# Kernel optimization log

Hardware: AMD Instinct MI355X
Metric: run time of the kernel (lower is better)

Reference implementation:

```python
import jax, jax.numpy as jnp
import numpy as np

N, E, G = 65536, 524288, 1024
ND, ED, HID, H, C = 21, 12, 128, 4, 32
L = 8  # num_blocks * 2 conv layers
EPS = 1e-5


def _gatv2(x, src, dst, ea, Wl, Wr, We, att, bias):
    # PyG GATv2Conv: xl=lin_l(x) (source), xr=lin_r(x) (target)
    n = x.shape[0]
    xl = jnp.einsum('nd,dhc->nhc', x, Wl)   # [N,H,C]
    xr = jnp.einsum('nd,dhc->nhc', x, Wr)
    el = jnp.einsum('ed,dhc->ehc', ea, We)  # [E,H,C]
    m = xl[src] + xr[dst] + el              # per-edge message pre-activation
    e = jnp.einsum('ehc,hc->eh', jax.nn.leaky_relu(m, 0.2), att)  # [E,H]
    # scatter softmax over incoming edges of each dst node
    emax = jax.ops.segment_max(e, dst, num_segments=n)
    emax = jnp.where(jnp.isfinite(emax), emax, 0.0)
    p = jnp.exp(e - emax[dst])
    denom = jax.ops.segment_sum(p, dst, num_segments=n)
    alpha = p / jnp.clip(denom, 1e-16)[dst]
    out = jax.ops.segment_sum(alpha[..., None] * xl[src], dst, num_segments=n)
    return out.reshape(n, H * C) + bias


def _bn(x, scale, bias):
    mu = x.mean(0)
    var = x.var(0)
    return (x - mu) * jax.lax.rsqrt(var + EPS) * scale + bias


def setup_inputs():
    key = jax.random.key(0)
    ks = jax.random.split(key, 16)
    f = lambda k, shp, s=0.05: jax.random.normal(k, shp, jnp.float32) * s
    return dict(
        x=f(ks[0], (N, ND), 1.0),
        edge_attr=f(ks[1], (E, ED), 1.0),
        edge_index=jax.random.randint(ks[2], (2, E), 0, N),
        batch=jnp.sort(jax.random.randint(ks[3], (N,), 0, G)),
        Win=f(ks[4], (ND, HID)), bin_=jnp.zeros(HID),
        Wl=f(ks[5], (L, HID, H, C)), Wr=f(ks[6], (L, HID, H, C)),
        We=f(ks[7], (L, ED, H, C)), att=f(ks[8], (L, H, C)),
        bconv=jnp.zeros((L, HID)),
        bn_scale=jnp.ones((L, HID)), bn_bias=jnp.zeros((L, HID)),
        Wv1=f(ks[9], (HID, 64)), bv1=jnp.zeros(64),
        Wv2=f(ks[10], (64, 3)), bv2=jnp.zeros(3),
        Wp1=f(ks[11], (2 * HID + ED, 64)), bp1=jnp.zeros(64),
        Wp2=f(ks[12], (64, 1)), bp2=jnp.zeros(1),
    )


def reference(x, edge_attr, edge_index, batch, Win, bin_, Wl, Wr, We, att,
              bconv, bn_scale, bn_bias, Wv1, bv1, Wv2, bv2, Wp1, bp1, Wp2, bp2):
    src0, dst0 = edge_index[0], edge_index[1]
    # add_self_loops with fill_value='mean' for edge features
    ones_e = jnp.ones((E,), x.dtype)
    deg = jax.ops.segment_sum(ones_e, dst0, num_segments=N)
    mean_ea = jax.ops.segment_sum(edge_attr, dst0, num_segments=N) / jnp.clip(deg, 1.0)[:, None]
    ar = jnp.arange(N)
    src = jnp.concatenate([src0, ar])
    dst = jnp.concatenate([dst0, ar])
    ea = jnp.concatenate([edge_attr, mean_ea], axis=0)

    h = jax.nn.relu(x @ Win + bin_)
    for b in range(L // 2):
        i, j = 2 * b, 2 * b + 1
        res = h
        h = _gatv2(h, src, dst, ea, Wl[i], Wr[i], We[i], att[i], bconv[i])
        h = jax.nn.relu(_bn(h, bn_scale[i], bn_bias[i]))
        h = _gatv2(h, src, dst, ea, Wl[j], Wr[j], We[j], att[j], bconv[j])
        h = _bn(h, bn_scale[j], bn_bias[j])
        h = jax.nn.relu(h + res)

    counts = jax.ops.segment_sum(jnp.ones((N,), h.dtype), batch, num_segments=G)
    pooled = jax.ops.segment_sum(h, batch, num_segments=G) / jnp.clip(counts, 1.0)[:, None]
    value_logits = jax.nn.relu(pooled @ Wv1 + bv1) @ Wv2 + bv2  # [G,3]

    edge_input = jnp.concatenate([h[src0], h[dst0], edge_attr], axis=1)  # [E, 2*HID+ED]
    policy_logits = (jax.nn.relu(edge_input @ Wp1 + bp1) @ Wp2 + bp2)[:, 0]  # [E]
    return value_logits, policy_logits
```

## Files before the change

### kernel.cpp

```cpp
#include <hip/hip_runtime.h>
#include <hip/hip_fp16.h>

#define NN 65536
#define EE 524288
#define EPX 589824
#define GG 1024
#define NSLOT 32

typedef __attribute__((ext_vector_type(8))) short bf16x8;
typedef __attribute__((ext_vector_type(4))) float f32x4;

#define LOG2E 1.44269504088896f


__device__ __forceinline__ unsigned short f2bf(float x) {
    unsigned int u = __float_as_uint(x);
    u += 0x7FFFu + ((u >> 16) & 1u);
    return (unsigned short)(u >> 16);
}
__device__ __forceinline__ float bflo(unsigned int w) { return __uint_as_float(w << 16); }
__device__ __forceinline__ float bfhi(unsigned int w) { return __uint_as_float(w & 0xFFFF0000u); }
__device__ __forceinline__ float bf2f(unsigned short u) { return __uint_as_float((unsigned int)u << 16); }
__device__ __forceinline__ float lrelu(float x) { return fmaf(0.4f, fabsf(x), 0.6f * x); }
__device__ __forceinline__ unsigned int packh2(float a, float b) {
    __half2 h = __floats2half2_rn(a, b);
    return *reinterpret_cast<unsigned int*>(&h);
}
__device__ __forceinline__ unsigned long long rfl64(unsigned long long v) {
    unsigned int lo = __builtin_amdgcn_readfirstlane((unsigned int)v);
    unsigned int hi = __builtin_amdgcn_readfirstlane((unsigned int)(v >> 32));
    return (((unsigned long long)hi) << 32) | lo;
}


__launch_bounds__(256)
__global__ void k_deg(const int* __restrict__ dst0, int* __restrict__ deg)
{
    int e = blockIdx.x * 256 + threadIdx.x;
    if (e >= EE) return;
    atomicAdd(&deg[dst0[e]], 1);
}

__launch_bounds__(1024)
__global__ void k_scan(const int* __restrict__ deg, int* __restrict__ rowptr)
{
    __shared__ int sums[1024];
    int t = threadIdx.x;
    int base = t * 64;
    int s = 0;
    for (int i = 0; i < 64; i++) s += deg[base + i] + 1;
    sums[t] = s;
    __syncthreads();
    for (int off = 1; off < 1024; off <<= 1) {
        int v = (t >= off) ? sums[t - off] : 0;
        __syncthreads();
        sums[t] += v;
        __syncthreads();
    }
    int off = sums[t] - s;
    for (int i = 0; i < 64; i++) { rowptr[base + i] = off; off += deg[base + i] + 1; }
    if (t == 1023) rowptr[NN] = off;
}

__launch_bounds__(256)
__global__ void k_scatter(const int* __restrict__ src0, const int* __restrict__ dst0,
                          const float* __restrict__ eattr,
                          const int* __restrict__ rowptr, const int* __restrict__ deg,
                          int* __restrict__ fill, int* __restrict__ csr_src,
                          unsigned short* __restrict__ eaCSR)
{
    int e = blockIdx.x * 256 + threadIdx.x;
    if (e >= EPX) return;
    if (e < EE) {
        int d = dst0[e];
        int pos = rowptr[d] + atomicAdd(&fill[d], 1);
        csr_src[pos] = src0[e] << 8;
        const float* ep = eattr + (size_t)e * 12;
        float4 a = *reinterpret_cast<const float4*>(ep);
        float4 b = *reinterpret_cast<const float4*>(ep + 4);
        float4 c = *reinterpret_cast<const float4*>(ep + 8);
        uint2* q = reinterpret_cast<uint2*>(eaCSR + (size_t)pos * 12);
        q[0] = make_uint2(packh2(a.x, a.y), packh2(a.z, a.w));
        q[1] = make_uint2(packh2(b.x, b.y), packh2(b.z, b.w));
        q[2] = make_uint2(packh2(c.x, c.y), packh2(c.z, c.w));
    } else {
        int n = e - EE;
        csr_src[rowptr[n] + deg[n]] = n << 8;
    }
}

__launch_bounds__(256)
__global__ void k_selfattr(const int* __restrict__ rowptr, unsigned short* __restrict__ eaCSR)
{
    int tid = blockIdx.x * 256 + threadIdx.x;
    int n = tid >> 4;
    int lk = tid & 15;
    if (lk >= 12) return;
    int beg = rowptr[n], endm1 = rowptr[n + 1] - 1;
    float s = 0.f;
    for (int p = beg; p < endm1; ++p) {
        __half h = *reinterpret_cast<const __half*>(&eaCSR[(size_t)p * 12 + lk]);
        s += __half2float(h);
    }
    float dv = fmaxf((float)(endm1 - beg), 1.0f);
    __half ho = __float2half(s / dv);
    eaCSR[(size_t)endm1 * 12 + lk] = *reinterpret_cast<unsigned short*>(&ho);
}


__launch_bounds__(256)
__global__ void k_wprep(const float* __restrict__ Wl, const float* __restrict__ Wr,
                        const float* __restrict__ Wp1,
                        unsigned short* __restrict__ wg, unsigned short* __restrict__ wp)
{
    int tid = blockIdx.x * 256 + threadIdx.x;
    if (tid < 32768) {
        int l = tid >> 12;
        int r = tid & 4095;
        int kt = r >> 10, ct = (r >> 6) & 15, lane = r & 63;
        int kb = kt * 32 + (lane >> 4) * 8;
        int col = ct * 16 + (lane & 15);
        const float* W = (col < 128) ? (Wl + (size_t)l * 16384 + col)
                                     : (Wr + (size_t)l * 16384 + (col - 128));
        unsigned short* o = wg + (size_t)tid * 8;
#pragma unroll
        for (int j = 0; j < 8; j++) o[j] = f2bf(W[(size_t)(kb + j) * 128]);
    } else if (tid < 34816) {
        int r = tid - 32768;
        int kt = r >> 9, ct = (r >> 6) & 7, lane = r & 63;
        int kb = kt * 32 + (lane >> 4) * 8;
        int col = ct * 16 + (lane & 15);
        const float* W = (col < 64) ? (Wp1 + col) : (Wp1 + 128 * 64 + (col - 64));
        unsigned short* o = wp + (size_t)r * 8;
#pragma unroll
        for (int j = 0; j < 8; j++) o[j] = f2bf(W[(size_t)(kb + j) * 64]);
    }
}


__launch_bounds__(256)
__global__ void k_input(const float* __restrict__ x, const float* __restrict__ Win,
                        const float* __restrict__ bin, float* __restrict__ h)
{
    __shared__ float W[21 * 128];
    int t = threadIdx.x;
    for (int i = t; i < 21 * 128; i += 256) W[i] = Win[i];
    __syncthreads();
    int c = t & 127, sub = t >> 7;
    int n0 = blockIdx.x * 16;
    float bc = bin[c];
    for (int i = 0; i < 8; i++) {
        int n = n0 + sub + i * 2;
        const float* xp = x + (size_t)n * 21;
        float acc = bc;
#pragma unroll
        for (int k = 0; k < 21; k++) acc = fmaf(xp[k], W[k * 128 + c], acc);
        h[(size_t)n * 128 + c] = fmaxf(acc, 0.f);
    }
}


__device__ __forceinline__ void load_afrag(const float* __restrict__ A, int arow, int kb,
                                           bf16x8 af[4])
{
#pragma unroll
    for (int kt = 0; kt < 4; kt++) {
        const float* ap = A + (size_t)arow * 128 + kt * 32 + kb;
        float4 lo = *reinterpret_cast<const float4*>(ap);
        float4 hi = *reinterpret_cast<const float4*>(ap + 4);
        bf16x8 v;
        v[0] = (short)f2bf(lo.x); v[1] = (short)f2bf(lo.y);
        v[2] = (short)f2bf(lo.z); v[3] = (short)f2bf(lo.w);
        v[4] = (short)f2bf(hi.x); v[5] = (short)f2bf(hi.y);
        v[6] = (short)f2bf(hi.z); v[7] = (short)f2bf(hi.w);
        af[kt] = v;
    }
}

__device__ __forceinline__ void gemm_gat_core(const bf16x8 af[4], const unsigned short* __restrict__ Bf,
                                              int row0, unsigned short* __restrict__ Cl,
                                              unsigned short* __restrict__ Cr, int lane)
{
    int crow = row0 + (lane >> 4) * 4;
    int c0 = lane & 15;
#pragma unroll
    for (int ct = 0; ct < 16; ct++) {
        f32x4 acc = {0.f, 0.f, 0.f, 0.f};
#pragma unroll
        for (int kt = 0; kt < 4; kt++) {
            bf16x8 bf = *reinterpret_cast<const bf16x8*>(Bf + ((size_t)(kt * 16 + ct) * 64 + lane) * 8);
            acc = __builtin_amdgcn_mfma_f32_16x16x32_bf16(af[kt], bf, acc, 0, 0, 0);
        }
        int col = ct * 16 + c0;
        unsigned short* C = (col < 128) ? Cl : Cr;
        int cc = col & 127;
#pragma unroll
        for (int r = 0; r < 4; r++)
            C[(size_t)(crow + r) * 128 + cc] = f2bf(acc[r]);
    }
}

__launch_bounds__(256)
__global__ void k_gemm_gat(const float* __restrict__ A, const unsigned short* __restrict__ Bf,
                           unsigned short* __restrict__ Cl, unsigned short* __restrict__ Cr)
{
    int wave = threadIdx.x >> 6, lane = threadIdx.x & 63;
    int row0 = blockIdx.x * 64 + wave * 16;
    bf16x8 af[4];
    load_afrag(A, row0 + (lane & 15), (lane >> 4) * 8, af);
    gemm_gat_core(af, Bf, row0, Cl, Cr, lane);
}

__launch_bounds__(256)
__global__ void k_gemm_gat_bn(const float* __restrict__ G, const float* __restrict__ bnstat,
                              const float* __restrict__ scale, const float* __restrict__ bias,
                              const unsigned short* __restrict__ Bf,
                              unsigned short* __restrict__ Cl, unsigned short* __restrict__ Cr)
{
    __shared__ float sA[128], bA[128];
    int t = threadIdx.x;
    if (t < 128) {
        float sum = 0.f, sq = 0.f;
#pragma unroll
        for (int sl = 0; sl < NSLOT; sl++) {
            sum += bnstat[sl * 256 + t];
            sq  += bnstat[sl * 256 + 128 + t];
        }
        const float invN = 1.0f / (float)NN;
        float mean = sum * invN;
        float var  = sq * invN - mean * mean;
        float sc   = scale[t] * rsqrtf(var + 1e-5f);
        sA[t] = sc;
        bA[t] = bias[t] - mean * sc;
    }
    __syncthreads();
    int wave = t >> 6, lane = t & 63;
    int row0 = blockIdx.x * 64 + wave * 16;
    int arow = row0 + (lane & 15);
    int kb = (lane >> 4) * 8;
    bf16x8 af[4];
#pragma unroll
    for (int kt = 0; kt < 4; kt++) {
        int cb = kt * 32 + kb;
        const float* gp = G + (size_t)arow * 128 + cb;
        float4 lo = *reinterpret_cast<const float4*>(gp);
        float4 hi = *reinterpret_cast<const float4*>(gp + 4);
        bf16x8 v;
        v[0] = (short)f2bf(fmaxf(fmaf(lo.x, sA[cb + 0], bA[cb + 0]), 0.f));
        v[1] = (short)f2bf(fmaxf(fmaf(lo.y, sA[cb + 1], bA[cb + 1]), 0.f));
        v[2] = (short)f2bf(fmaxf(fmaf(lo.z, sA[cb + 2], bA[cb + 2]), 0.f));
        v[3] = (short)f2bf(fmaxf(fmaf(lo.w, sA[cb + 3], bA[cb + 3]), 0.f));
        v[4] = (short)f2bf(fmaxf(fmaf(hi.x, sA[cb + 4], bA[cb + 4]), 0.f));
        v[5] = (short)f2bf(fmaxf(fmaf(hi.y, sA[cb + 5], bA[cb + 5]), 0.f));
        v[6] = (short)f2bf(fmaxf(fmaf(hi.z, sA[cb + 6], bA[cb + 6]), 0.f));
        v[7] = (short)f2bf(fmaxf(fmaf(hi.w, sA[cb + 7], bA[cb + 7]), 0.f));
        af[kt] = v;
    }
    gemm_gat_core(af, Bf, row0, Cl, Cr, lane);
}

__launch_bounds__(256)
__global__ void k_gemm_pol(const float* __restrict__ A, const unsigned short* __restrict__ Bf,
                           unsigned short* __restrict__ P)
{
    int wave = threadIdx.x >> 6, lane = threadIdx.x & 63;
    int row0 = blockIdx.x * 64 + wave * 16;
    bf16x8 af[4];
    load_afrag(A, row0 + (lane & 15), (lane >> 4) * 8, af);
    int crow = row0 + (lane >> 4) * 4;
    int c0 = lane & 15;
#pragma unroll
    for (int ct = 0; ct < 8; ct++) {
        f32x4 acc = {0.f, 0.f, 0.f, 0.f};
#pragma unroll
        for (int kt = 0; kt < 4; kt++) {
            bf16x8 bf = *reinterpret_cast<const bf16x8*>(Bf + ((size_t)(kt * 8 + ct) * 64 + lane) * 8);
            acc = __builtin_amdgcn_mfma_f32_16x16x32_bf16(af[kt], bf, acc, 0, 0, 0);
        }
        int col = ct * 16 + c0;
#pragma unroll
        for (int r = 0; r < 4; r++)
            P[(size_t)(crow + r) * 128 + col] = f2bf(acc[r]);
    }
}


__device__ __forceinline__ float2 edge_el(uint2 qa, uint2 qb, uint2 qc,
                                          const __half2 wx[6], const __half2 wy[6])
{
    __half2 e0 = *reinterpret_cast<const __half2*>(&qa.x);
    __half2 e1 = *reinterpret_cast<const __half2*>(&qa.y);
    __half2 e2 = *reinterpret_cast<const __half2*>(&qb.x);
    __half2 e3 = *reinterpret_cast<const __half2*>(&qb.y);
    __half2 e4 = *reinterpret_cast<const __half2*>(&qc.x);
    __half2 e5 = *reinterpret_cast<const __half2*>(&qc.y);
    __half2 ax = __hmul2(e0, wx[0]);
    ax = __hfma2(e1, wx[1], ax); ax = __hfma2(e2, wx[2], ax);
    ax = __hfma2(e3, wx[3], ax); ax = __hfma2(e4, wx[4], ax);
    ax = __hfma2(e5, wx[5], ax);
    __half2 ay = __hmul2(e0, wy[0]);
    ay = __hfma2(e1, wy[1], ay); ay = __hfma2(e2, wy[2], ay);
    ay = __hfma2(e3, wy[3], ay); ay = __hfma2(e4, wy[4], ay);
    ay = __hfma2(e5, wy[5], ay);
    float2 r;
    r.x = __half2float(__hadd(__low2half(ax), __high2half(ax)));
    r.y = __half2float(__hadd(__low2half(ay), __high2half(ay)));
    return r;
}

__device__ __forceinline__ float head_reduce(float t)
{
    t += __shfl_xor(t, 1);
    t += __shfl_xor(t, 2);
    t += __shfl_xor(t, 4);
    t += __shfl_xor(t, 8);
    return t;
}

__launch_bounds__(256)
__global__ void k_gat(const unsigned short* __restrict__ xlb, const unsigned short* __restrict__ xrb,
                      const unsigned short* __restrict__ eaCSR,
                      const int* __restrict__ rowptr, const int* __restrict__ csr_src,
                      const float* __restrict__ We, const float* __restrict__ att,
                      const float* __restrict__ bconv, float* __restrict__ g,
                      float* __restrict__ bnstat)
{
    int wid = blockIdx.x * 4 + (threadIdx.x >> 6);
    int lane = threadIdx.x & 63;
    int f0 = lane * 2;

    const int* cs_s = (const int*)rfl64((unsigned long long)csr_src);
    const unsigned short* ea_s = (const unsigned short*)rfl64((unsigned long long)eaCSR);

    __half2 wx[6], wy[6];
#pragma unroll
    for (int j = 0; j < 6; j++) {
        float2 w0 = *reinterpret_cast<const float2*>(We + (2 * j) * 128 + f0);
        float2 w1 = *reinterpret_cast<const float2*>(We + (2 * j + 1) * 128 + f0);
        wx[j] = __floats2half2_rn(w0.x, w1.x);
        wy[j] = __floats2half2_rn(w0.y, w1.y);
    }
    float2 av = *reinterpret_cast<const float2*>(att + f0);
    av.x *= LOG2E; av.y *= LOG2E;
    float2 bc = *reinterpret_cast<const float2*>(bconv + f0);
    const char* xl_lane = reinterpret_cast<const char*>(xlb) + (lane << 2);

    float bs0 = 0.f, bs1 = 0.f, bq0 = 0.f, bq1 = 0.f;

    for (int n = wid * 4; n < wid * 4 + 4; ++n) {
        unsigned int xrw = *reinterpret_cast<const unsigned int*>(xrb + (size_t)n * 128 + f0);
        float xr0 = bflo(xrw), xr1 = bfhi(xrw);

        float m = -INFINITY, s = 0.f, a0 = 0.f, a1 = 0.f;
        int beg = rowptr[n], end = rowptr[n + 1];
        int idx = beg;
        for (; idx + 4 <= end; idx += 4) {
            int off0 = cs_s[idx],     off1 = cs_s[idx + 1];
            int off2 = cs_s[idx + 2], off3 = cs_s[idx + 3];
            const uint2* q = reinterpret_cast<const uint2*>(ea_s + (size_t)idx * 12);
            uint2 qa = q[0], qb = q[1],  qc = q[2];
            uint2 ra = q[3], rb = q[4],  rc = q[5];
            uint2 sa = q[6], sb = q[7],  sc = q[8];
            uint2 ta = q[9], tb = q[10], tc = q[11];
            unsigned int xw0 = *reinterpret_cast<const unsigned int*>(xl_lane + off0);
            unsigned int xw1 = *reinterpret_cast<const unsigned int*>(xl_lane + off1);
            unsigned int xw2 = *reinterpret_cast<const unsigned int*>(xl_lane + off2);
            unsigned int xw3 = *reinterpret_cast<const unsigned int*>(xl_lane + off3);

            float2 el0 = edge_el(qa, qb, qc, wx, wy);
            float2 el1 = edge_el(ra, rb, rc, wx, wy);
            float2 el2 = edge_el(sa, sb, sc, wx, wy);
            float2 el3 = edge_el(ta, tb, tc, wx, wy);

            float xa0 = bflo(xw0), xa1 = bfhi(xw0);
            float xb0 = bflo(xw1), xb1 = bfhi(xw1);
            float xc0 = bflo(xw2), xc1 = bfhi(xw2);
            float xd0 = bflo(xw3), xd1 = bfhi(xw3);

            float t0 = lrelu(xa0 + xr0 + el0.x) * av.x + lrelu(xa1 + xr1 + el0.y) * av.y;
            float t1 = lrelu(xb0 + xr0 + el1.x) * av.x + lrelu(xb1 + xr1 + el1.y) * av.y;
            float t2 = lrelu(xc0 + xr0 + el2.x) * av.x + lrelu(xc1 + xr1 + el2.y) * av.y;
            float t3 = lrelu(xd0 + xr0 + el3.x) * av.x + lrelu(xd1 + xr1 + el3.y) * av.y;
            t0 = head_reduce(t0); t1 = head_reduce(t1);
            t2 = head_reduce(t2); t3 = head_reduce(t3);

            float nm = fmaxf(fmaxf(fmaxf(t0, t1), fmaxf(t2, t3)), m);
            float so = exp2f(m - nm);
            float w0 = exp2f(t0 - nm);
            float w1 = exp2f(t1 - nm);
            float w2 = exp2f(t2 - nm);
            float w3 = exp2f(t3 - nm);
            s  = fmaf(s, so, (w0 + w1) + (w2 + w3));
            a0 = fmaf(a0, so, fmaf(w0, xa0, fmaf(w1, xb0, fmaf(w2, xc0, w3 * xd0))));
            a1 = fmaf(a1, so, fmaf(w0, xa1, fmaf(w1, xb1, fmaf(w2, xc1, w3 * xd1))));
            m = nm;
        }
        for (; idx < end; ++idx) {
            int off0 = cs_s[idx];
            const uint2* q = reinterpret_cast<const uint2*>(ea_s + (size_t)idx * 12);
            uint2 qa = q[0], qb = q[1], qc = q[2];
            unsigned int xw0 = *reinterpret_cast<const unsigned int*>(xl_lane + off0);
            float2 el0 = edge_el(qa, qb, qc, wx, wy);
            float xa0 = bflo(xw0), xa1 = bfhi(xw0);
            float tt = lrelu(xa0 + xr0 + el0.x) * av.x + lrelu(xa1 + xr1 + el0.y) * av.y;
            tt = head_reduce(tt);
            float nm = fmaxf(m, tt);
            float so = exp2f(m - nm);
            float w  = exp2f(tt - nm);
            s  = fmaf(s, so, w);
            a0 = fmaf(a0, so, w * xa0);
            a1 = fmaf(a1, so, w * xa1);
            m = nm;
        }
        float inv = 1.f / s;
        float r0 = fmaf(a0, inv, bc.x);
        float r1 = fmaf(a1, inv, bc.y);
        *reinterpret_cast<float2*>(g + (size_t)n * 128 + f0) = make_float2(r0, r1);
        bs0 += r0; bs1 += r1;
        bq0 = fmaf(r0, r0, bq0); bq1 = fmaf(r1, r1, bq1);
    }

    __shared__ float red[256 * 4];
    int t = threadIdx.x;
    red[t * 4 + 0] = bs0; red[t * 4 + 1] = bs1;
    red[t * 4 + 2] = bq0; red[t * 4 + 3] = bq1;
    __syncthreads();
    if (t < 64) {
        float v0 = red[t * 4 + 0] + red[(t + 64) * 4 + 0] + red[(t + 128) * 4 + 0] + red[(t + 192) * 4 + 0];
        float v1 = red[t * 4 + 1] + red[(t + 64) * 4 + 1] + red[(t + 128) * 4 + 1] + red[(t + 192) * 4 + 1];
        float q0 = red[t * 4 + 2] + red[(t + 64) * 4 + 2] + red[(t + 128) * 4 + 2] + red[(t + 192) * 4 + 2];
        float q1 = red[t * 4 + 3] + red[(t + 64) * 4 + 3] + red[(t + 128) * 4 + 3] + red[(t + 192) * 4 + 3];
        float* slot = bnstat + (size_t)(blockIdx.x & (NSLOT - 1)) * 256;
        atomicAdd(&slot[2 * t + 0], v0);
        atomicAdd(&slot[2 * t + 1], v1);
        atomicAdd(&slot[128 + 2 * t + 0], q0);
        atomicAdd(&slot[128 + 2 * t + 1], q1);
    }
}


__launch_bounds__(256)
__global__ void k_bnapply_res_relu(const float4* __restrict__ gin,
                                   const float* __restrict__ bnstat,
                                   const float* __restrict__ scale, const float* __restrict__ bias,
                                   float4* __restrict__ hbuf)
{
    __shared__ float sA[128], bA[128];
    int t = threadIdx.x;
    if (t < 128) {
        float sum = 0.f, sq = 0.f;
#pragma unroll
        for (int sl = 0; sl < NSLOT; sl++) {
            sum += bnstat[sl * 256 + t];
            sq  += bnstat[sl * 256 + 128 + t];
        }
        const float invN = 1.0f / (float)NN;
        float mean = sum * invN;
        float var  = sq * invN - mean * mean;
        float sc   = scale[t] * rsqrtf(var + 1e-5f);
        sA[t] = sc;
        bA[t] = bias[t] - mean * sc;
    }
    __syncthreads();
    int idx = blockIdx.x * 256 + t;
    int c4 = (idx & 31) * 4;
    float4 v = gin[idx];
    float4 hv = hbuf[idx];
    float4 r;
    r.x = fmaxf(fmaf(v.x, sA[c4 + 0], bA[c4 + 0]) + hv.x, 0.f);
    r.y = fmaxf(fmaf(v.y, sA[c4 + 1], bA[c4 + 1]) + hv.y, 0.f);
    r.z = fmaxf(fmaf(v.z, sA[c4 + 2], bA[c4 + 2]) + hv.z, 0.f);
    r.w = fmaxf(fmaf(v.w, sA[c4 + 3], bA[c4 + 3]) + hv.w, 0.f);
    hbuf[idx] = r;
}


__launch_bounds__(128)
__global__ void k_pool(const float* __restrict__ h, const int* __restrict__ batch,
                       float* __restrict__ pooled, float* __restrict__ cnt)
{
    int c = threadIdx.x;
    int r0 = blockIdx.x * 128;
    int cur = batch[r0];
    float acc = 0.f;
    float run = 0.f;
    for (int i = 0; i < 128; ++i) {
        int r = r0 + i;
        int b = batch[r];
        if (b != cur) {
            atomicAdd(&pooled[(size_t)cur * 128 + c], acc);
            if (c == 0) atomicAdd(&cnt[cur], run);
            acc = 0.f; run = 0.f; cur = b;
        }
        acc += h[(size_t)r * 128 + c];
        run += 1.f;
    }
    atomicAdd(&pooled[(size_t)cur * 128 + c], acc);
    if (c == 0) atomicAdd(&cnt[cur], run);
}

__launch_bounds__(64)
__global__ void k_value(const float* __restrict__ pooled, const float* __restrict__ cnt,
                        const float* __restrict__ Wv1, const float* __restrict__ bv1,
                        const float* __restrict__ Wv2, const float* __restrict__ bv2,
                        float* __restrict__ out)
{
    int gi = blockIdx.x;
    int l = threadIdx.x;
    float inv = 1.f / fmaxf(cnt[gi], 1.f);
    const float* pr = pooled + (size_t)gi * 128;
    float z = bv1[l];
    for (int k = 0; k < 128; k++) z = fmaf(pr[k] * inv, Wv1[k * 64 + l], z);
    z = fmaxf(z, 0.f);
#pragma unroll
    for (int j = 0; j < 3; j++) {
        float p = z * Wv2[l * 3 + j];
        p += __shfl_xor(p, 32); p += __shfl_xor(p, 16); p += __shfl_xor(p, 8);
        p += __shfl_xor(p, 4);  p += __shfl_xor(p, 2);  p += __shfl_xor(p, 1);
        if (l == 0) out[gi * 3 + j] = p + bv2[j];
    }
}


__launch_bounds__(256)
__global__ void k_policy(const unsigned short* __restrict__ P,
                         const float* __restrict__ eattr,
                         const int* __restrict__ src0, const int* __restrict__ dst0,
                         const float* __restrict__ Wp1c, const float* __restrict__ bp1,
                         const float* __restrict__ Wp2, const float* __restrict__ bp2,
                         float* __restrict__ out)
{
    int wave = (blockIdx.x * 256 + threadIdx.x) >> 6;
    int lane = threadIdx.x & 63;
    const float* ea_s = (const float*)rfl64((unsigned long long)eattr);
    const int* s_s = (const int*)rfl64((unsigned long long)src0);
    const int* d_s = (const int*)rfl64((unsigned long long)dst0);
    float w1c[12];
#pragma unroll
    for (int k = 0; k < 12; k++) w1c[k] = Wp1c[k * 64 + lane];
    float wp2 = Wp2[lane];
    float bb = bp1[lane];
    float b2 = bp2[0];
    for (int i = 0; i < 8; i++) {
        int e = wave * 8 + i;
        int sI = s_s[e], dI = d_s[e];
        const float* ep = ea_s + (size_t)e * 12;
        float4 e0 = *reinterpret_cast<const float4*>(ep);
        float4 e1 = *reinterpret_cast<const float4*>(ep + 4);
        float4 e2 = *reinterpret_cast<const float4*>(ep + 8);
        float z = bf2f(P[(size_t)sI * 128 + lane]) + bf2f(P[(size_t)dI * 128 + 64 + lane]) + bb;
        z += e0.x * w1c[0] + e0.y * w1c[1] + e0.z * w1c[2]  + e0.w * w1c[3]
           + e1.x * w1c[4] + e1.y * w1c[5] + e1.z * w1c[6]  + e1.w * w1c[7]
           + e2.x * w1c[8] + e2.y * w1c[9] + e2.z * w1c[10] + e2.w * w1c[11];
        z = fmaxf(z, 0.f);
        float p = z * wp2;
        p += __shfl_xor(p, 32); p += __shfl_xor(p, 16); p += __shfl_xor(p, 8);
        p += __shfl_xor(p, 4);  p += __shfl_xor(p, 2);  p += __shfl_xor(p, 1);
        if (lane == 0) out[3072 + e] = p + b2;
    }
}


extern "C" void kernel_launch(void* const* d_in, const int* in_sizes, int n_in,
                              void* d_out, int out_size, void* d_ws, size_t ws_size,
                              hipStream_t stream)
{
    const float* x     = (const float*)d_in[0];
    const float* eattr = (const float*)d_in[1];
    const int*   eidx  = (const int*)d_in[2];
    const int*   batch = (const int*)d_in[3];
    const float* Win   = (const float*)d_in[4];
    const float* bin   = (const float*)d_in[5];
    const float* Wl    = (const float*)d_in[6];
    const float* Wr    = (const float*)d_in[7];
    const float* We    = (const float*)d_in[8];
    const float* att   = (const float*)d_in[9];
    const float* bconv = (const float*)d_in[10];
    const float* bnsc  = (const float*)d_in[11];
    const float* bnbi  = (const float*)d_in[12];
    const float* Wv1   = (const float*)d_in[13];
    const float* bv1   = (const float*)d_in[14];
    const float* Wv2   = (const float*)d_in[15];
    const float* bv2   = (const float*)d_in[16];
    const float* Wp1   = (const float*)d_in[17];
    const float* bp1   = (const float*)d_in[18];
    const float* Wp2   = (const float*)d_in[19];
    const float* bp2   = (const float*)d_in[20];
    float* out = (float*)d_out;

    const int* src0 = eidx;
    const int* dst0 = eidx + EE;

    const size_t NH = (size_t)NN * 128;
    float* ws = (float*)d_ws;
    float* h  = ws;
    float* g  = h + NH;
    unsigned short* xlb = (unsigned short*)(g + NH);
    unsigned short* xrb = xlb + NH;
    unsigned short* eaCSR = xrb + NH;
    int* rowptr = (int*)(eaCSR + (size_t)EPX * 12);
    int* csr_src = rowptr + (NN + 1);
    int* deg  = csr_src + EPX;
    int* fill = deg + NN;
    float* bnstat = (float*)(fill + NN);
    float* pooled = bnstat + 8 * NSLOT * 256;
    float* cnt    = pooled + (size_t)GG * 128;
    size_t zero_elems = (size_t)NN + NN + 8 * NSLOT * 256 + (size_t)GG * 128 + GG;
    unsigned short* wg = (unsigned short*)(cnt + GG);
    unsigned short* wp = wg + 8 * 32768;

    hipMemsetAsync(deg, 0, zero_elems * sizeof(float), stream);

    k_deg<<<EE / 256, 256, 0, stream>>>(dst0, deg);
    k_scan<<<1, 1024, 0, stream>>>(deg, rowptr);
    k_scatter<<<EPX / 256, 256, 0, stream>>>(src0, dst0, eattr, rowptr, deg, fill, csr_src, eaCSR);
    k_selfattr<<<(NN * 16) / 256, 256, 0, stream>>>(rowptr, eaCSR);
    k_wprep<<<136, 256, 0, stream>>>(Wl, Wr, Wp1, wg, wp);

    k_input<<<NN / 16, 256, 0, stream>>>(x, Win, bin, h);

    for (int l = 0; l < 8; l++) {
        float* bs = bnstat + (size_t)l * NSLOT * 256;
        if (l % 2 == 0) {
            k_gemm_gat<<<NN / 64, 256, 0, stream>>>(h, wg + (size_t)l * 32768, xlb, xrb);
        } else {
            float* bsp = bnstat + (size_t)(l - 1) * NSLOT * 256;
            k_gemm_gat_bn<<<NN / 64, 256, 0, stream>>>(g, bsp,
                                                       bnsc + (size_t)(l - 1) * 128,
                                                       bnbi + (size_t)(l - 1) * 128,
                                                       wg + (size_t)l * 32768, xlb, xrb);
        }
        k_gat<<<NN / 16, 256, 0, stream>>>(xlb, xrb, eaCSR, rowptr, csr_src,
                                           We + (size_t)l * 1536, att + (size_t)l * 128,
                                           bconv + (size_t)l * 128, g, bs);
        if (l % 2 == 1) {
            k_bnapply_res_relu<<<(NN * 128 / 4) / 256, 256, 0, stream>>>(
                (const float4*)g, bs, bnsc + (size_t)l * 128, bnbi + (size_t)l * 128,
                (float4*)h);
        }
    }

    k_pool<<<NN / 128, 128, 0, stream>>>(h, batch, pooled, cnt);
    k_value<<<GG, 64, 0, stream>>>(pooled, cnt, Wv1, bv1, Wv2, bv2, out);

    unsigned short* P = xlb;
    k_gemm_pol<<<NN / 64, 256, 0, stream>>>(h, wp, P);
    k_policy<<<NN / 4, 256, 0, stream>>>(P, eattr, src0, dst0,
                                         Wp1 + 256 * 64, bp1, Wp2, bp2, out);
}
```

Before: 1.146 ms.

## Split GAT layer into edge-parallel logit kernel and node-parallel aggregation kernel

Moves the per-edge attention logit computation into its own edge-parallel kernel, where each wave handles a fixed chunk of 64 CSR edges and writes per-head logits to a scratch buffer. The aggregation kernel then reads precomputed logits and only gathers source features for the online softmax. The aim is to remove the load imbalance that variable node degree causes in the fused per-node loop. In exchange it adds a csr_dst array, a second gather of xl per edge, an extra launch, and a logit write plus read-back each layer.

Measured after the change: 1.246 ms. 1.09x slower.

```diff
diff --git a/kernel.cpp b/kernel.cpp
--- a/kernel.cpp
+++ b/kernel.cpp
@@ -67,7 +67,7 @@
                           const float* __restrict__ eattr,
                           const int* __restrict__ rowptr, const int* __restrict__ deg,
                           int* __restrict__ fill, int* __restrict__ csr_src,
-                          unsigned short* __restrict__ eaCSR)
+                          int* __restrict__ csr_dst, unsigned short* __restrict__ eaCSR)
 {
     int e = blockIdx.x * 256 + threadIdx.x;
     if (e >= EPX) return;
@@ -75,6 +75,7 @@
         int d = dst0[e];
         int pos = rowptr[d] + atomicAdd(&fill[d], 1);
         csr_src[pos] = src0[e] << 8;
+        csr_dst[pos] = d << 8;
         const float* ep = eattr + (size_t)e * 12;
         float4 a = *reinterpret_cast<const float4*>(ep);
         float4 b = *reinterpret_cast<const float4*>(ep + 4);
@@ -85,7 +86,9 @@
         q[2] = make_uint2(packh2(c.x, c.y), packh2(c.z, c.w));
     } else {
         int n = e - EE;
-        csr_src[rowptr[n] + deg[n]] = n << 8;
+        int pos = rowptr[n] + deg[n];
+        csr_src[pos] = n << 8;
+        csr_dst[pos] = n << 8;
     }
 }
 
@@ -318,19 +321,17 @@
 }
 
 __launch_bounds__(256)
-__global__ void k_gat(const unsigned short* __restrict__ xlb, const unsigned short* __restrict__ xrb,
-                      const unsigned short* __restrict__ eaCSR,
-                      const int* __restrict__ rowptr, const int* __restrict__ csr_src,
-                      const float* __restrict__ We, const float* __restrict__ att,
-                      const float* __restrict__ bconv, float* __restrict__ g,
-                      float* __restrict__ bnstat)
+__global__ void k_logit(const unsigned short* __restrict__ xlb, const unsigned short* __restrict__ xrb,
+                        const unsigned short* __restrict__ eaCSR,
+                        const int* __restrict__ csr_src, const int* __restrict__ csr_dst,
+                        const float* __restrict__ We, const float* __restrict__ att,
+                        float* __restrict__ tlog)
 {
     int wid = blockIdx.x * 4 + (threadIdx.x >> 6);
     int lane = threadIdx.x & 63;
     int f0 = lane * 2;
-
-    const int* cs_s = (const int*)rfl64((unsigned long long)csr_src);
-    const unsigned short* ea_s = (const unsigned short*)rfl64((unsigned long long)eaCSR);
+    int head = lane >> 4;
+    bool wl = (lane & 15) == 0;
 
     __half2 wx[6], wy[6];
 #pragma unroll
@@ -342,47 +343,83 @@
     }
     float2 av = *reinterpret_cast<const float2*>(att + f0);
     av.x *= LOG2E; av.y *= LOG2E;
+    const char* xl_lane = reinterpret_cast<const char*>(xlb) + (lane << 2);
+    const char* xr_lane = reinterpret_cast<const char*>(xrb) + (lane << 2);
+
+    int p0 = wid * 64;
+    for (int p = p0; p < p0 + 64; p += 4) {
+        int so0 = csr_src[p],     so1 = csr_src[p + 1];
+        int so2 = csr_src[p + 2], so3 = csr_src[p + 3];
+        int do0 = csr_dst[p],     do1 = csr_dst[p + 1];
+        int do2 = csr_dst[p + 2], do3 = csr_dst[p + 3];
+        const uint2* q = reinterpret_cast<const uint2*>(eaCSR + (size_t)p * 12);
+        uint2 qa = q[0], qb = q[1],  qc = q[2];
+        uint2 ra = q[3], rb = q[4],  rc = q[5];
+        uint2 sa = q[6], sb = q[7],  sc = q[8];
+        uint2 ta = q[9], tb = q[10], tc = q[11];
+        unsigned int xs0 = *reinterpret_cast<const unsigned int*>(xl_lane + so0);
+        unsigned int xs1 = *reinterpret_cast<const unsigned int*>(xl_lane + so1);
+        unsigned int xs2 = *reinterpret_cast<const unsigned int*>(xl_lane + so2);
+        unsigned int xs3 = *reinterpret_cast<const unsigned int*>(xl_lane + so3);
+        unsigned int xd0 = *reinterpret_cast<const unsigned int*>(xr_lane + do0);
+        unsigned int xd1 = *reinterpret_cast<const unsigned int*>(xr_lane + do1);
+        unsigned int xd2 = *reinterpret_cast<const unsigned int*>(xr_lane + do2);
+        unsigned int xd3 = *reinterpret_cast<const unsigned int*>(xr_lane + do3);
+
+        float2 el0 = edge_el(qa, qb, qc, wx, wy);
+        float2 el1 = edge_el(ra, rb, rc, wx, wy);
+        float2 el2 = edge_el(sa, sb, sc, wx, wy);
+        float2 el3 = edge_el(ta, tb, tc, wx, wy);
+
+        float t0 = lrelu(bflo(xs0) + bflo(xd0) + el0.x) * av.x + lrelu(bfhi(xs0) + bfhi(xd0) + el0.y) * av.y;
+        float t1 = lrelu(bflo(xs1) + bflo(xd1) + el1.x) * av.x + lrelu(bfhi(xs1) + bfhi(xd1) + el1.y) * av.y;
+        float t2 = lrelu(bflo(xs2) + bflo(xd2) + el2.x) * av.x + lrelu(bfhi(xs2) + bfhi(xd2) + el2.y) * av.y;
+        float t3 = lrelu(bflo(xs3) + bflo(xd3) + el3.x) * av.x + lrelu(bfhi(xs3) + bfhi(xd3) + el3.y) * av.y;
+        t0 = head_reduce(t0); t1 = head_reduce(t1);
+        t2 = head_reduce(t2); t3 = head_reduce(t3);
+
+        if (wl) {
+            tlog[(size_t)(p + 0) * 4 + head] = t0;
+            tlog[(size_t)(p + 1) * 4 + head] = t1;
+            tlog[(size_t)(p + 2) * 4 + head] = t2;
+            tlog[(size_t)(p + 3) * 4 + head] = t3;
+        }
+    }
+}
+
+
+__launch_bounds__(256)
+__global__ void k_gat2(const unsigned short* __restrict__ xlb,
+                       const float* __restrict__ tlog,
+                       const int* __restrict__ rowptr, const int* __restrict__ csr_src,
+                       const float* __restrict__ bconv, float* __restrict__ g,
+                       float* __restrict__ bnstat)
+{
+    int wid = blockIdx.x * 4 + (threadIdx.x >> 6);
+    int lane = threadIdx.x & 63;
+    int f0 = lane * 2;
+    int head = lane >> 4;
     float2 bc = *reinterpret_cast<const float2*>(bconv + f0);
     const char* xl_lane = reinterpret_cast<const char*>(xlb) + (lane << 2);
+    const float* tl = tlog + head;
 
     float bs0 = 0.f, bs1 = 0.f, bq0 = 0.f, bq1 = 0.f;
 
     for (int n = wid * 4; n < wid * 4 + 4; ++n) {
-        unsigned int xrw = *reinterpret_cast<const unsigned int*>(xrb + (size_t)n * 128 + f0);
-        float xr0 = bflo(xrw), xr1 = bfhi(xrw);
-
         float m = -INFINITY, s = 0.f, a0 = 0.f, a1 = 0.f;
         int beg = rowptr[n], end = rowptr[n + 1];
         int idx = beg;
         for (; idx + 4 <= end; idx += 4) {
-            int off0 = cs_s[idx],     off1 = cs_s[idx + 1];
-            int off2 = cs_s[idx + 2], off3 = cs_s[idx + 3];
-            const uint2* q = reinterpret_cast<const uint2*>(ea_s + (size_t)idx * 12);
-            uint2 qa = q[0], qb = q[1],  qc = q[2];
-            uint2 ra = q[3], rb = q[4],  rc = q[5];
-            uint2 sa = q[6], sb = q[7],  sc = q[8];
-            uint2 ta = q[9], tb = q[10], tc = q[11];
+            int off0 = csr_src[idx],     off1 = csr_src[idx + 1];
+            int off2 = csr_src[idx + 2], off3 = csr_src[idx + 3];
+            float t0 = tl[(size_t)(idx + 0) * 4];
+            float t1 = tl[(size_t)(idx + 1) * 4];
+            float t2 = tl[(size_t)(idx + 2) * 4];
+            float t3 = tl[(size_t)(idx + 3) * 4];
             unsigned int xw0 = *reinterpret_cast<const unsigned int*>(xl_lane + off0);
             unsigned int xw1 = *reinterpret_cast<const unsigned int*>(xl_lane + off1);
             unsigned int xw2 = *reinterpret_cast<const unsigned int*>(xl_lane + off2);
             unsigned int xw3 = *reinterpret_cast<const unsigned int*>(xl_lane + off3);
-
-            float2 el0 = edge_el(qa, qb, qc, wx, wy);
-            float2 el1 = edge_el(ra, rb, rc, wx, wy);
-            float2 el2 = edge_el(sa, sb, sc, wx, wy);
-            float2 el3 = edge_el(ta, tb, tc, wx, wy);
-
-            float xa0 = bflo(xw0), xa1 = bfhi(xw0);
-            float xb0 = bflo(xw1), xb1 = bfhi(xw1);
-            float xc0 = bflo(xw2), xc1 = bfhi(xw2);
-            float xd0 = bflo(xw3), xd1 = bfhi(xw3);
-
-            float t0 = lrelu(xa0 + xr0 + el0.x) * av.x + lrelu(xa1 + xr1 + el0.y) * av.y;
-            float t1 = lrelu(xb0 + xr0 + el1.x) * av.x + lrelu(xb1 + xr1 + el1.y) * av.y;
-            float t2 = lrelu(xc0 + xr0 + el2.x) * av.x + lrelu(xc1 + xr1 + el2.y) * av.y;
-            float t3 = lrelu(xd0 + xr0 + el3.x) * av.x + lrelu(xd1 + xr1 + el3.y) * av.y;
-            t0 = head_reduce(t0); t1 = head_reduce(t1);
-            t2 = head_reduce(t2); t3 = head_reduce(t3);
 
             float nm = fmaxf(fmaxf(fmaxf(t0, t1), fmaxf(t2, t3)), m);
             float so = exp2f(m - nm);
@@ -390,23 +427,23 @@
             float w1 = exp2f(t1 - nm);
             float w2 = exp2f(t2 - nm);
             float w3 = exp2f(t3 - nm);
+            float xa0 = bflo(xw0), xa1 = bfhi(xw0);
+            float xb0 = bflo(xw1), xb1 = bfhi(xw1);
+            float xc0 = bflo(xw2), xc1 = bfhi(xw2);
+            float xd0 = bflo(xw3), xd1 = bfhi(xw3);
             s  = fmaf(s, so, (w0 + w1) + (w2 + w3));
             a0 = fmaf(a0, so, fmaf(w0, xa0, fmaf(w1, xb0, fmaf(w2, xc0, w3 * xd0))));
             a1 = fmaf(a1, so, fmaf(w0, xa1, fmaf(w1, xb1, fmaf(w2, xc1, w3 * xd1))));
             m = nm;
         }
         for (; idx < end; ++idx) {
-            int off0 = cs_s[idx];
-            const uint2* q = reinterpret_cast<const uint2*>(ea_s + (size_t)idx * 12);
-            uint2 qa = q[0], qb = q[1], qc = q[2];
+            int off0 = csr_src[idx];
+            float tt = tl[(size_t)idx * 4];
             unsigned int xw0 = *reinterpret_cast<const unsigned int*>(xl_lane + off0);
-            float2 el0 = edge_el(qa, qb, qc, wx, wy);
-            float xa0 = bflo(xw0), xa1 = bfhi(xw0);
-            float tt = lrelu(xa0 + xr0 + el0.x) * av.x + lrelu(xa1 + xr1 + el0.y) * av.y;
-            tt = head_reduce(tt);
             float nm = fmaxf(m, tt);
             float so = exp2f(m - nm);
             float w  = exp2f(tt - nm);
+            float xa0 = bflo(xw0), xa1 = bfhi(xw0);
             s  = fmaf(s, so, w);
             a0 = fmaf(a0, so, w * xa0);
             a1 = fmaf(a1, so, w * xa1);
@@ -600,7 +637,8 @@
     unsigned short* eaCSR = xrb + NH;
     int* rowptr = (int*)(eaCSR + (size_t)EPX * 12);
     int* csr_src = rowptr + (NN + 1);
-    int* deg  = csr_src + EPX;
+    int* csr_dst = csr_src + EPX;
+    int* deg  = csr_dst + EPX;
     int* fill = deg + NN;
     float* bnstat = (float*)(fill + NN);
     float* pooled = bnstat + 8 * NSLOT * 256;
@@ -608,12 +646,14 @@
     size_t zero_elems = (size_t)NN + NN + 8 * NSLOT * 256 + (size_t)GG * 128 + GG;
     unsigned short* wg = (unsigned short*)(cnt + GG);
     unsigned short* wp = wg + 8 * 32768;
+    float* tlog = (float*)(wp + 16384);
 
     hipMemsetAsync(deg, 0, zero_elems * sizeof(float), stream);
 
     k_deg<<<EE / 256, 256, 0, stream>>>(dst0, deg);
     k_scan<<<1, 1024, 0, stream>>>(deg, rowptr);
-    k_scatter<<<EPX / 256, 256, 0, stream>>>(src0, dst0, eattr, rowptr, deg, fill, csr_src, eaCSR);
+    k_scatter<<<EPX / 256, 256, 0, stream>>>(src0, dst0, eattr, rowptr, deg, fill,
+                                             csr_src, csr_dst, eaCSR);
     k_selfattr<<<(NN * 16) / 256, 256, 0, stream>>>(rowptr, eaCSR);
     k_wprep<<<136, 256, 0, stream>>>(Wl, Wr, Wp1, wg, wp);
 
@@ -630,9 +670,11 @@
                                                        bnbi + (size_t)(l - 1) * 128,
                                                        wg + (size_t)l * 32768, xlb, xrb);
         }
-        k_gat<<<NN / 16, 256, 0, stream>>>(xlb, xrb, eaCSR, rowptr, csr_src,
-                                           We + (size_t)l * 1536, att + (size_t)l * 128,
-                                           bconv + (size_t)l * 128, g, bs);
+        k_logit<<<EPX / 256, 256, 0, stream>>>(xlb, xrb, eaCSR, csr_src, csr_dst,
+                                               We + (size_t)l * 1536, att + (size_t)l * 128,
+                                               tlog);
+        k_gat2<<<NN / 16, 256, 0, stream>>>(xlb, tlog, rowptr, csr_src,
+                                            bconv + (size_t)l * 128, g, bs);
         if (l % 2 == 1) {
             k_bnapply_res_relu<<<(NN * 128 / 4) / 256, 256, 0, stream>>>(
                 (const float4*)g, bs, bnsc + (size_t)l * 128, bnbi + (size_t)l * 128,
```
